# Kernel optimization log

Hardware: AMD Instinct MI355X
Metric: run time of the kernel (lower is better)

Reference implementation:

```python
import jax, jax.numpy as jnp
import numpy as np


def setup_inputs() -> dict:
    key = jax.random.key(0)
    kK, kV, kQ, kP, kA = jax.random.split(key, 5)
    b, d, N, T = 16, 512, 1024, 2048
    K = jax.random.normal(kK, (b, d, N), dtype=jnp.float32)
    V = jax.random.normal(kV, (b, d, N), dtype=jnp.float32)
    Q = jax.random.normal(kQ, (b, d, T), dtype=jnp.float32)
    previous_position = jax.random.randint(kP, (b,), 0, N)
    # previous attention: a valid attention matrix (softmax over N)
    previous_att = jax.nn.softmax(jax.random.uniform(kA, (b, N, T), dtype=jnp.float32), axis=1)
    return {
        "K": K,
        "V": V,
        "Q": Q,
        "force_incremental": 1,   # static python int -> bool branch
        "previous_position": previous_position,
        "previous_att": previous_att,
        "current_time": 1024,     # static python int timestep
    }


def reference(K, V, Q, force_incremental, previous_position, previous_att, current_time):
    # K, V: [b, d, N]; Q: [b, d, T]
    d = Q.shape[1]
    scale = 1.0 / np.sqrt(d)  # Config.d == feature dim
    # A: [b, N, T], softmax over N (text axis)
    A = jax.nn.softmax(jnp.einsum('bdn,bdt->bnt', K, Q) * scale, axis=1)
    current_position = jnp.argmax(A[:, :, current_time], axis=1)  # [b]
    if force_incremental:
        N = A.shape[1]
        # restore already-committed alignment prefix
        A = A.at[:, :, :current_time].set(previous_att[:, :, :current_time])
        difference = current_position - previous_position
        force_needed = (difference < -1) | (difference > 3)  # [b]
        # delta: one-hot at previous_position+1 (scatter_ of ones collapses to one-hot)
        idx = jnp.clip(previous_position + 1, 0, N - 1)
        delta = jax.nn.one_hot(idx, N, dtype=A.dtype)  # [b, N]
        col = jnp.where(force_needed[:, None], delta, A[:, :, current_time])
        A = A.at[:, :, current_time].set(col)
        current_position = jnp.argmax(col, axis=1)
    # R: [b, d, T]
    R = jnp.einsum('bdn,bnt->bdt', V, A)
    return A, R, current_position
```

## Files before the change

kernel.cpp:

```cpp
#include <hip/hip_runtime.h>
#include <hip/hip_bf16.h>

#define B_  16
#define D_  512
#define N_  1024
#define T_  2048
#define CT_ 1024
#define SCALE 0.04419417382415922f

typedef __attribute__((ext_vector_type(8))) short bf16x8;
typedef __attribute__((ext_vector_type(4))) float f32x4;
typedef __attribute__((ext_vector_type(8))) unsigned short u16x8;

#define GLDS16(g, l) __builtin_amdgcn_global_load_lds( \
    (const __attribute__((address_space(1))) unsigned int*)(g), \
    (__attribute__((address_space(3))) unsigned int*)(l), 16, 0, 0)

__device__ __forceinline__ unsigned short f2bf(float f) {
    union { float f; unsigned u; } v; v.f = f;
    unsigned r = v.u + 0x7fffu + ((v.u >> 16) & 1u);
    return (unsigned short)(r >> 16);
}
__device__ __forceinline__ float bf2f(unsigned short s) {
    union { unsigned u; float f; } v; v.u = ((unsigned)s) << 16;
    return v.f;
}


__global__ __launch_bounds__(256) void prep_all(
    const float* __restrict__ K, const float* __restrict__ Q,
    const float* __restrict__ V, const float* __restrict__ prev_att,
    unsigned short* __restrict__ KT, unsigned short* __restrict__ QT,
    unsigned short* __restrict__ Vbf, float* __restrict__ A,
    unsigned short* __restrict__ PbfT, float* __restrict__ invsum,
    float* __restrict__ colS) {
    __shared__ float tl[64][65];
    __shared__ float qv_s[64];
    __shared__ float red[256];
    const int bid = blockIdx.x;
    const int tid = threadIdx.x;
    const int rr = tid >> 4, cc = (tid & 15) * 4;

    if (bid < 4096) {
        const int nx = bid & 15, rem = bid >> 4;
        const int ty_ = rem & 15, b = rem >> 4;
        const int n0 = nx * 64, t0 = ty_ * 64;
        const float* ib = prev_att + (long)b * N_ * T_;
        float* Ab = A + (long)b * N_ * T_;
        unsigned short* ob = PbfT + (long)b * T_ * N_;
        f32x4 v[4];
#pragma unroll
        for (int p = 0; p < 4; ++p)
            v[p] = __builtin_nontemporal_load(
                (const f32x4*)&ib[(long)(n0 + p * 16 + rr) * T_ + t0 + cc]);
#pragma unroll
        for (int p = 0; p < 4; ++p)
            __builtin_nontemporal_store(
                v[p], (f32x4*)&Ab[(long)(n0 + p * 16 + rr) * T_ + t0 + cc]);
#pragma unroll
        for (int p = 0; p < 4; ++p) {
            tl[p*16+rr][cc] = v[p][0]; tl[p*16+rr][cc+1] = v[p][1];
            tl[p*16+rr][cc+2] = v[p][2]; tl[p*16+rr][cc+3] = v[p][3];
        }
        __syncthreads();
#pragma unroll
        for (int p = 0; p < 4; ++p) {
            int c = p * 16 + rr;
            ushort4 w;
            w.x = f2bf(tl[cc+0][c]); w.y = f2bf(tl[cc+1][c]);
            w.z = f2bf(tl[cc+2][c]); w.w = f2bf(tl[cc+3][c]);
            *(ushort4*)&ob[(long)(t0 + c) * N_ + n0 + cc] = w;
        }
    } else if (bid < 6144) {
        const int r = bid - 4096;
        const int rx = r & 7, rem = r >> 3;
        const int cy = rem & 15, b = rem >> 4;
        const int r0 = rx * 64, c0 = cy * 64;
        const float* ib = K + (long)b * D_ * N_;
        unsigned short* ob = KT + (long)b * 1024 * 512;
        if (tid < 64)
            qv_s[tid] = __builtin_nontemporal_load(
                &Q[((long)b * D_ + r0 + tid) * T_ + CT_]);
        f32x4 v[4];
#pragma unroll
        for (int p = 0; p < 4; ++p)
            v[p] = __builtin_nontemporal_load(
                (const f32x4*)&ib[(long)(r0 + p * 16 + rr) * N_ + c0 + cc]);
#pragma unroll
        for (int p = 0; p < 4; ++p) {
            tl[p*16+rr][cc] = v[p][0]; tl[p*16+rr][cc+1] = v[p][1];
            tl[p*16+rr][cc+2] = v[p][2]; tl[p*16+rr][cc+3] = v[p][3];
        }
        __syncthreads();
#pragma unroll
        for (int p = 0; p < 4; ++p) {
            int c = p * 16 + rr;
            ushort4 w;
            w.x = f2bf(tl[cc+0][c]); w.y = f2bf(tl[cc+1][c]);
            w.z = f2bf(tl[cc+2][c]); w.w = f2bf(tl[cc+3][c]);
            *(ushort4*)&ob[(long)(c0 + c) * 512 + r0 + cc] = w;
        }
        {
            const int n = tid & 63, g = tid >> 6;
            float p = 0.f;
#pragma unroll
            for (int j = 0; j < 16; ++j)
                p += tl[g * 16 + j][n] * qv_s[g * 16 + j];
            red[tid] = p;
            __syncthreads();
            if (tid < 64)
                atomicAdd(&colS[(long)b * N_ + c0 + tid],
                          red[tid] + red[64 + tid] + red[128 + tid] + red[192 + tid]);
        }
    } else if (bid < 8192) {
        const int r = bid - 6144;
        const int rx = r & 7, rem = r >> 3;
        const int cy = rem & 15, b = rem >> 4;
        const int r0 = rx * 64, c0 = cy * 64;
        const float* ib = Q + (long)b * D_ * T_;
        unsigned short* ob = QT + (long)b * 1024 * 512;
        f32x4 v[4];
#pragma unroll
        for (int p = 0; p < 4; ++p)
            v[p] = __builtin_nontemporal_load(
                (const f32x4*)&ib[(long)(r0 + p * 16 + rr) * T_ + CT_ + c0 + cc]);
#pragma unroll
        for (int p = 0; p < 4; ++p) {
            tl[p*16+rr][cc] = v[p][0]; tl[p*16+rr][cc+1] = v[p][1];
            tl[p*16+rr][cc+2] = v[p][2]; tl[p*16+rr][cc+3] = v[p][3];
        }
        __syncthreads();
#pragma unroll
        for (int p = 0; p < 4; ++p) {
            int c = p * 16 + rr;
            ushort4 w;
            w.x = f2bf(tl[cc+0][c]); w.y = f2bf(tl[cc+1][c]);
            w.z = f2bf(tl[cc+2][c]); w.w = f2bf(tl[cc+3][c]);
            *(ushort4*)&ob[(long)(c0 + c) * 512 + r0 + cc] = w;
        }
    } else if (bid < 9216) {
        const long total = (long)B_ * D_ * N_ / 4;
        for (long i = (long)(bid - 8192) * 256 + tid; i < total; i += 1024L * 256) {
            f32x4 v = __builtin_nontemporal_load(&((const f32x4*)V)[i]);
            ushort4 w;
            w.x = f2bf(v[0]); w.y = f2bf(v[1]); w.z = f2bf(v[2]); w.w = f2bf(v[3]);
            ((ushort4*)Vbf)[i] = w;
        }
    } else {
        const int idx = (bid - 9216) * 256 + tid;
        const int b = idx >> 10, t = idx & 1023;
        invsum[(long)b * T_ + t] = 1.0f;
    }
}

__global__ __launch_bounds__(256) void score_gemm_fused(
    const unsigned short* __restrict__ KT, const unsigned short* __restrict__ QT,
    unsigned short* __restrict__ PbfT, float* __restrict__ partial) {
    const int wg = blockIdx.x;
    const int b  = wg >> 6;
    const int rem = wg & 63;
    const int by = rem >> 3;
    const int bx = rem & 7;
    const int m0 = by * 128;
    const int t0 = bx * 128;
    __shared__ __align__(16) unsigned short buf[128 * 136];
    __shared__ float csum[2][128];
    unsigned short* sA = buf;
    unsigned short* sB = buf + 128 * 64;
    const int tid = threadIdx.x, lane = tid & 63, wave = tid >> 6;
    const int wm = wave >> 1, wn = wave & 1;
    const int lq = lane & 15, half = lane >> 4;
    const int srow = tid >> 3;
    const int cin  = tid & 7;

    const unsigned short* Ab = KT + (long)b * N_ * 512;
    const unsigned short* Bb = QT + (long)b * N_ * 512;

    f32x4 acc[4][4];
#pragma unroll
    for (int i = 0; i < 4; ++i)
#pragma unroll
        for (int j = 0; j < 4; ++j) acc[i][j] = f32x4{0.f, 0.f, 0.f, 0.f};

    for (int k0 = 0; k0 < 512; k0 += 64) {
#pragma unroll
        for (int c = 0; c < 4; ++c) {
            const int row  = c * 32 + srow;
            const int clog = cin ^ (row & 7);
            GLDS16(Ab + (long)(m0 + row) * 512 + k0 + clog * 8,
                   &sA[(c * 256 + wave * 64) * 8]);
            GLDS16(Bb + (long)(t0 + row) * 512 + k0 + clog * 8,
                   &sB[(c * 256 + wave * 64) * 8]);
        }
        __syncthreads();
#pragma unroll
        for (int kk = 0; kk < 2; ++kk) {
            bf16x8 af[4], bfr[4];
#pragma unroll
            for (int mi = 0; mi < 4; ++mi) {
                const int row = wm * 64 + mi * 16 + lq;
                af[mi] = *(const bf16x8*)&sA[row * 64 + (((kk * 4 + half) ^ (row & 7)) * 8)];
            }
#pragma unroll
            for (int ni = 0; ni < 4; ++ni) {
                const int row = wn * 64 + ni * 16 + lq;
                bfr[ni] = *(const bf16x8*)&sB[row * 64 + (((kk * 4 + half) ^ (row & 7)) * 8)];
            }
#pragma unroll
            for (int mi = 0; mi < 4; ++mi)
#pragma unroll
                for (int ni = 0; ni < 4; ++ni)
                    acc[mi][ni] = __builtin_amdgcn_mfma_f32_16x16x32_bf16(
                        af[mi], bfr[ni], acc[mi][ni], 0, 0, 0);
        }
        __syncthreads();
    }

#pragma unroll
    for (int mi = 0; mi < 4; ++mi)
#pragma unroll
        for (int ni = 0; ni < 4; ++ni)
#pragma unroll
            for (int r = 0; r < 4; ++r)
                acc[mi][ni][r] = __expf(acc[mi][ni][r] * SCALE);

    float cp[4];
#pragma unroll
    for (int ni = 0; ni < 4; ++ni) {
        float s = 0.f;
#pragma unroll
        for (int mi = 0; mi < 4; ++mi)
#pragma unroll
            for (int r = 0; r < 4; ++r) s += acc[mi][ni][r];
        s += __shfl_xor(s, 16);
        s += __shfl_xor(s, 32);
        cp[ni] = s;
    }

#pragma unroll
    for (int mi = 0; mi < 4; ++mi)
#pragma unroll
        for (int ni = 0; ni < 4; ++ni) {
            const int col = wn * 64 + ni * 16 + lq;
            const int row = wm * 64 + mi * 16 + half * 4;
            ushort4 w;
            w.x = f2bf(acc[mi][ni][0]); w.y = f2bf(acc[mi][ni][1]);
            w.z = f2bf(acc[mi][ni][2]); w.w = f2bf(acc[mi][ni][3]);
            *(ushort4*)&buf[col * 136 + row] = w;
        }
    if (lane < 16) {
#pragma unroll
        for (int ni = 0; ni < 4; ++ni)
            csum[wm][wn * 64 + ni * 16 + lane] = cp[ni];
    }
    __syncthreads();

    if (tid < 128)
        partial[((long)b * 8 + by) * 1024 + t0 + tid] =
            csum[0][tid] + csum[1][tid];

    unsigned short* ob = PbfT + (long)b * T_ * N_;
#pragma unroll
    for (int p = 0; p < 8; ++p) {
        const int idx = tid + p * 256;
        const int row = idx >> 4, ch = idx & 15;
        u16x8 w = *(const u16x8*)&buf[row * 136 + ch * 8];
        *(u16x8*)&ob[(long)(CT_ + t0 + row) * N_ + m0 + ch * 8] = w;
    }
}

__global__ __launch_bounds__(256) void emitA_inv(
    const unsigned short* __restrict__ PbfT, float* __restrict__ A,
    const float* __restrict__ partial, float* __restrict__ invsum) {
    const int b   = blockIdx.z;
    const int n0  = blockIdx.x * 64;
    const int tc0 = blockIdx.y * 128;
    __shared__ float tl[128][65];
    __shared__ float inv_s[128];
    const int tid = threadIdx.x;
    if (tid < 128) {
        float s = 0.f;
#pragma unroll
        for (int k = 0; k < 8; ++k) s += partial[((long)b * 8 + k) * 1024 + tc0 + tid];
        const float iv = 1.f / s;
        inv_s[tid] = iv;
        if (blockIdx.x == 0) invsum[(long)b * T_ + CT_ + tc0 + tid] = iv;
    }
    __syncthreads();
    const unsigned short* Pb = PbfT + (long)b * T_ * N_;
    float* Ab = A + (long)b * N_ * T_;
    const int rr = tid >> 4, cc = (tid & 15) * 4;
#pragma unroll
    for (int p = 0; p < 8; ++p) {
        const int row = p * 16 + rr;
        ushort4 w = *(const ushort4*)&Pb[(long)(CT_ + tc0 + row) * N_ + n0 + cc];
        const float inv = inv_s[row];
        tl[row][cc]   = bf2f(w.x) * inv; tl[row][cc+1] = bf2f(w.y) * inv;
        tl[row][cc+2] = bf2f(w.z) * inv; tl[row][cc+3] = bf2f(w.w) * inv;
    }
    __syncthreads();
    const int rr2 = tid >> 5, cc2 = (tid & 31) * 4;
#pragma unroll
    for (int p = 0; p < 8; ++p) {
        const int c = p * 8 + rr2;
        f32x4 o;
        o[0] = tl[cc2+0][c]; o[1] = tl[cc2+1][c];
        o[2] = tl[cc2+2][c]; o[3] = tl[cc2+3][c];
        __builtin_nontemporal_store(o, (f32x4*)&Ab[(long)(n0 + c) * T_ + CT_ + tc0 + cc2]);
    }
}

__global__ __launch_bounds__(256) void r_gemm_new(
    const unsigned short* __restrict__ Vbf, const unsigned short* __restrict__ PbfT,
    const float* __restrict__ invsum, float* __restrict__ R) {
    const int wg = blockIdx.x;
    const int b  = wg >> 6;
    const int rem = wg & 63;
    const int by = rem >> 4;
    const int bx = rem & 15;
    const int m0  = by * 128;
    const int nn0 = bx * 128;
    __shared__ __align__(16) unsigned short sA[128 * 64];
    __shared__ __align__(16) unsigned short sB[128 * 64];
    const int tid = threadIdx.x, lane = tid & 63, wave = tid >> 6;
    const int wm = wave >> 1, wn = wave & 1;
    const int lq = lane & 15, half = lane >> 4;
    const int srow = tid >> 3;
    const int cin  = tid & 7;

    const unsigned short* Ab = Vbf  + (long)b * D_ * N_;
    const unsigned short* Bb = PbfT + (long)b * T_ * N_;

    f32x4 acc[4][4];
#pragma unroll
    for (int i = 0; i < 4; ++i)
#pragma unroll
        for (int j = 0; j < 4; ++j) acc[i][j] = f32x4{0.f, 0.f, 0.f, 0.f};

    for (int k0 = 0; k0 < 1024; k0 += 64) {
#pragma unroll
        for (int c = 0; c < 4; ++c) {
            const int row  = c * 32 + srow;
            const int clog = cin ^ (row & 7);
            GLDS16(Ab + (long)(m0  + row) * 1024 + k0 + clog * 8,
                   &sA[(c * 256 + wave * 64) * 8]);
            GLDS16(Bb + (long)(nn0 + row) * 1024 + k0 + clog * 8,
                   &sB[(c * 256 + wave * 64) * 8]);
        }
        __syncthreads();
#pragma unroll
        for (int kk = 0; kk < 2; ++kk) {
            bf16x8 af[4], bfr[4];
#pragma unroll
            for (int mi = 0; mi < 4; ++mi) {
                const int row = wm * 64 + mi * 16 + lq;
                af[mi] = *(const bf16x8*)&sA[row * 64 + (((kk * 4 + half) ^ (row & 7)) * 8)];
            }
#pragma unroll
            for (int ni = 0; ni < 4; ++ni) {
                const int row = wn * 64 + ni * 16 + lq;
                bfr[ni] = *(const bf16x8*)&sB[row * 64 + (((kk * 4 + half) ^ (row & 7)) * 8)];
            }
#pragma unroll
            for (int mi = 0; mi < 4; ++mi)
#pragma unroll
                for (int ni = 0; ni < 4; ++ni)
                    acc[mi][ni] = __builtin_amdgcn_mfma_f32_16x16x32_bf16(
                        af[mi], bfr[ni], acc[mi][ni], 0, 0, 0);
        }
        __syncthreads();
    }
    float* Rb = R + (long)b * D_ * T_;
#pragma unroll
    for (int ni = 0; ni < 4; ++ni) {
        const int col = nn0 + wn * 64 + ni * 16 + lq;
        const float inv = invsum[(long)b * T_ + col];
#pragma unroll
        for (int mi = 0; mi < 4; ++mi)
#pragma unroll
            for (int r = 0; r < 4; ++r) {
                const int row = m0 + wm * 64 + mi * 16 + half * 4 + r;
                __builtin_nontemporal_store(acc[mi][ni][r] * inv,
                                            &Rb[(long)row * T_ + col]);
            }
    }
}

__global__ void col_scores_fp32(const float* __restrict__ K, const float* __restrict__ Q,
                                float* __restrict__ A) {
    const int b  = blockIdx.y;
    const int n0 = blockIdx.x * 128;
    const int tid = threadIdx.x;
    const int nl = tid & 127, dh = tid >> 7;
    __shared__ float qv[D_];
    __shared__ float part[256];
    for (int d = tid; d < D_; d += 256) qv[d] = Q[((long)b * D_ + d) * T_ + CT_];
    __syncthreads();
    float acc = 0.f;
    const float* Kb = K + (long)b * D_ * N_;
    for (int d = dh * 256; d < dh * 256 + 256; ++d)
        acc += Kb[(long)d * N_ + n0 + nl] * qv[d];
    part[tid] = acc;
    __syncthreads();
    if (tid < 128) {
        float s = (part[tid] + part[tid + 128]) * SCALE;
        A[((long)b * N_ + n0 + nl) * T_ + CT_] = s;
    }
}

__global__ void finalize_col(float* __restrict__ A, unsigned short* __restrict__ abfT,
                             float* __restrict__ invsum, const float* __restrict__ colS,
                             float* __restrict__ pos_out,
                             const int* __restrict__ prev_pos,
                             const int* __restrict__ force_p) {
    const int force = *force_p;
    const int b = blockIdx.x;
    const int tid = threadIdx.x;
    float* Ab = A + (long)b * N_ * T_;
    __shared__ float s[N_];
    __shared__ float redf[256];
    __shared__ int   redi[256];

    if (colS) {
        for (int n = tid; n < N_; n += 256) s[n] = colS[(long)b * N_ + n] * SCALE;
    } else {
        for (int n = tid; n < N_; n += 256) s[n] = Ab[(long)n * T_ + CT_];
    }
    __syncthreads();

    float m = -1e30f;
    for (int n = tid; n < N_; n += 256) m = fmaxf(m, s[n]);
    redf[tid] = m; __syncthreads();
    for (int w = 128; w > 0; w >>= 1) {
        if (tid < w) redf[tid] = fmaxf(redf[tid], redf[tid + w]);
        __syncthreads();
    }
    m = redf[0];
    __syncthreads();

    float sum = 0.f;
    for (int n = tid; n < N_; n += 256) sum += __expf(s[n] - m);
    redf[tid] = sum; __syncthreads();
    for (int w = 128; w > 0; w >>= 1) {
        if (tid < w) redf[tid] += redf[tid + w];
        __syncthreads();
    }
    sum = redf[0];
    __syncthreads();

    int idxl = N_;
    for (int n = tid; n < N_; n += 256) if (s[n] == m && n < idxl) idxl = n;
    redi[tid] = idxl; __syncthreads();
    for (int w = 128; w > 0; w >>= 1) {
        if (tid < w) redi[tid] = min(redi[tid], redi[tid + w]);
        __syncthreads();
    }
    const int cpos = redi[0];

    const int prev = prev_pos[b];
    const int diff = cpos - prev;
    const int fneed = force && (diff < -1 || diff > 3);
    int oneidx = prev + 1;
    oneidx = oneidx < 0 ? 0 : (oneidx > N_ - 1 ? N_ - 1 : oneidx);
    const float inv = 1.f / sum;

    for (int n = tid; n < N_; n += 256) {
        float v = fneed ? (n == oneidx ? 1.f : 0.f) : __expf(s[n] - m) * inv;
        Ab[(long)n * T_ + CT_] = v;
        if (abfT) abfT[(long)b * T_ * N_ + (long)CT_ * N_ + n] = f2bf(v);
    }
    if (tid == 0) {
        if (invsum) invsum[(long)b * T_ + CT_] = 1.0f;
        pos_out[b] = (float)(fneed ? oneidx : cpos);
    }
}

__global__ void copy_prefix(const float* __restrict__ prev_att, float* __restrict__ A) {
    const int per_row = CT_ >> 2;
    const long total = (long)B_ * N_ * per_row;
    for (long i = (long)blockIdx.x * blockDim.x + threadIdx.x; i < total;
         i += (long)gridDim.x * blockDim.x) {
        long row = i / per_row;
        int  c4  = (int)(i - row * per_row);
        long off = row * T_ + (long)c4 * 4;
        *(float4*)(A + off) = *(const float4*)(prev_att + off);
    }
}

__global__ void softmax_part_old(const float* __restrict__ A, float* __restrict__ partial) {
    const int b  = blockIdx.z;
    const int n0 = blockIdx.y * 128;
    const int tx = threadIdx.x & 63, ty = threadIdx.x >> 6;
    const int ci = blockIdx.x * 64 + tx;
    const int t  = CT_ + ci;
    const float* Ab = A + (long)b * N_ * T_;
    float s = 0.f;
    for (int r = ty; r < 128; r += 4)
        s += __expf(Ab[(long)(n0 + r) * T_ + t] * SCALE);
    __shared__ float red2[4][64];
    red2[ty][tx] = s;
    __syncthreads();
    if (ty == 0) {
        float tot = red2[0][tx] + red2[1][tx] + red2[2][tx] + red2[3][tx];
        partial[((long)b * 8 + blockIdx.y) * 1024 + ci] = tot;
    }
}

__global__ __launch_bounds__(256) void score_gemm_old(
    const float* __restrict__ K, const float* __restrict__ Q, float* __restrict__ A) {
    const int b  = blockIdx.z;
    const int n0 = blockIdx.y * 128;
    const int t0 = blockIdx.x * 128;
    __shared__ __align__(16) unsigned short sK[128 * 40];
    __shared__ __align__(16) unsigned short sQ[128 * 40];
    const int tid = threadIdx.x;
    const int lane = tid & 63, wave = tid >> 6;
    const int wm = wave >> 1, wn = wave & 1;
    const int lq = lane & 15, half = lane >> 4;
    const int xl = tid & 127, grp = tid >> 7;
    f32x4 acc[4][4];
#pragma unroll
    for (int i = 0; i < 4; ++i)
#pragma unroll
        for (int j = 0; j < 4; ++j) acc[i][j] = f32x4{0.f, 0.f, 0.f, 0.f};
    const float* Kb = K + (long)b * D_ * N_;
    const float* Qb = Q + (long)b * D_ * T_;
    for (int d0 = 0; d0 < D_; d0 += 32) {
#pragma unroll
        for (int j = 0; j < 4; ++j) {
            ushort4 w;
#pragma unroll
            for (int i = 0; i < 4; ++i)
                ((unsigned short*)&w)[i] = f2bf(Kb[(long)(d0 + grp*16 + j*4 + i) * N_ + n0 + xl]);
            *(ushort4*)&sK[xl * 40 + grp * 16 + j * 4] = w;
        }
#pragma unroll
        for (int j = 0; j < 4; ++j) {
            ushort4 w;
#pragma unroll
            for (int i = 0; i < 4; ++i)
                ((unsigned short*)&w)[i] = f2bf(Qb[(long)(d0 + grp*16 + j*4 + i) * T_ + CT_ + t0 + xl]);
            *(ushort4*)&sQ[xl * 40 + grp * 16 + j * 4] = w;
        }
        __syncthreads();
        bf16x8 af[4], bfr[4];
#pragma unroll
        for (int mi = 0; mi < 4; ++mi)
            af[mi] = *(const bf16x8*)&sK[(wm * 64 + mi * 16 + lq) * 40 + half * 8];
#pragma unroll
        for (int ni = 0; ni < 4; ++ni)
            bfr[ni] = *(const bf16x8*)&sQ[(wn * 64 + ni * 16 + lq) * 40 + half * 8];
#pragma unroll
        for (int mi = 0; mi < 4; ++mi)
#pragma unroll
            for (int ni = 0; ni < 4; ++ni)
                acc[mi][ni] = __builtin_amdgcn_mfma_f32_16x16x32_bf16(
                    af[mi], bfr[ni], acc[mi][ni], 0, 0, 0);
        __syncthreads();
    }
    float* Ab = A + (long)b * N_ * T_;
#pragma unroll
    for (int mi = 0; mi < 4; ++mi)
#pragma unroll
        for (int ni = 0; ni < 4; ++ni) {
            const int col = CT_ + t0 + wn * 64 + ni * 16 + lq;
#pragma unroll
            for (int r = 0; r < 4; ++r)
                Ab[(long)(n0 + wm*64 + mi*16 + half*4 + r) * T_ + col] = acc[mi][ni][r];
        }
}

__global__ void softmax_scale_old(float* __restrict__ A, const float* __restrict__ partial) {
    const int b  = blockIdx.z;
    const int n0 = blockIdx.y * 256;
    const int tx = threadIdx.x & 63, ty = threadIdx.x >> 6;
    const int ci = blockIdx.x * 64 + tx;
    const int t  = CT_ + ci;
    float sum = 0.f;
#pragma unroll
    for (int k = 0; k < 8; ++k) sum += partial[((long)b * 8 + k) * 1024 + ci];
    const float inv = 1.f / sum;
    float* Ab = A + (long)b * N_ * T_;
    for (int r = ty; r < 256; r += 4) {
        long off = (long)(n0 + r) * T_ + t;
        Ab[off] = __expf(Ab[off] * SCALE) * inv;
    }
}

__global__ __launch_bounds__(256) void r_gemm_old(
    const float* __restrict__ V, const float* __restrict__ A, float* __restrict__ R) {
    const int b  = blockIdx.z;
    const int d0 = blockIdx.y * 128;
    const int t0 = blockIdx.x * 128;
    __shared__ __align__(16) unsigned short sV[128 * 40];
    __shared__ __align__(16) unsigned short sA2[128 * 40];
    const int tid = threadIdx.x;
    const int lane = tid & 63, wave = tid >> 6;
    const int wm = wave >> 1, wn = wave & 1;
    const int lq = lane & 15, half = lane >> 4;
    const int xl = tid & 127, grp = tid >> 7;
    const int vd = tid >> 3, vn4 = (tid & 7) * 4;
    f32x4 acc[4][4];
#pragma unroll
    for (int i = 0; i < 4; ++i)
#pragma unroll
        for (int j = 0; j < 4; ++j) acc[i][j] = f32x4{0.f, 0.f, 0.f, 0.f};
    const float* Vb = V + (long)b * D_ * N_;
    const float* Ab = A + (long)b * N_ * T_;
    for (int n0 = 0; n0 < N_; n0 += 32) {
#pragma unroll
        for (int p = 0; p < 4; ++p) {
            int dl = p * 32 + vd;
            float4 v = *(const float4*)&Vb[(long)(d0 + dl) * N_ + n0 + vn4];
            ushort4 w;
            w.x = f2bf(v.x); w.y = f2bf(v.y); w.z = f2bf(v.z); w.w = f2bf(v.w);
            *(ushort4*)&sV[dl * 40 + vn4] = w;
        }
#pragma unroll
        for (int j = 0; j < 4; ++j) {
            ushort4 w;
#pragma unroll
            for (int i = 0; i < 4; ++i)
                ((unsigned short*)&w)[i] = f2bf(Ab[(long)(n0 + grp*16 + j*4 + i) * T_ + t0 + xl]);
            *(ushort4*)&sA2[xl * 40 + grp * 16 + j * 4] = w;
        }
        __syncthreads();
        bf16x8 af[4], bfr[4];
#pragma unroll
        for (int mi = 0; mi < 4; ++mi)
            af[mi] = *(const bf16x8*)&sV[(wm * 64 + mi * 16 + lq) * 40 + half * 8];
#pragma unroll
        for (int ni = 0; ni < 4; ++ni)
            bfr[ni] = *(const bf16x8*)&sA2[(wn * 64 + ni * 16 + lq) * 40 + half * 8];
#pragma unroll
        for (int mi = 0; mi < 4; ++mi)
#pragma unroll
            for (int ni = 0; ni < 4; ++ni)
                acc[mi][ni] = __builtin_amdgcn_mfma_f32_16x16x32_bf16(
                    af[mi], bfr[ni], acc[mi][ni], 0, 0, 0);
        __syncthreads();
    }
    float* Rb = R + (long)b * D_ * T_;
#pragma unroll
    for (int mi = 0; mi < 4; ++mi)
#pragma unroll
        for (int ni = 0; ni < 4; ++ni) {
            const int col = t0 + wn * 64 + ni * 16 + lq;
#pragma unroll
            for (int r = 0; r < 4; ++r)
                Rb[(long)(d0 + wm*64 + mi*16 + half*4 + r) * T_ + col] = acc[mi][ni][r];
        }
}

extern "C" void kernel_launch(void* const* d_in, const int* in_sizes, int n_in,
                              void* d_out, int out_size, void* d_ws, size_t ws_size,
                              hipStream_t stream) {
    const float* K        = (const float*)d_in[0];
    const float* V        = (const float*)d_in[1];
    const float* Q        = (const float*)d_in[2];
    const int*   force_p  = (const int*)d_in[3];
    const int*   prev_pos = (const int*)d_in[4];
    const float* prev_att = (const float*)d_in[5];

    float* A       = (float*)d_out;
    float* R       = A + (long)B_ * N_ * T_;
    float* pos_out = R + (long)B_ * D_ * T_;

    const size_t oKT = 0;
    const size_t oQT = oKT + (size_t)B_ * N_ * D_ * 2;
    const size_t oV  = oQT + (size_t)B_ * N_ * D_ * 2;
    const size_t oPT = oV  + (size_t)B_ * D_ * N_ * 2;
    const size_t oP  = oPT + (size_t)B_ * T_ * N_ * 2;
    const size_t oI  = oP  + (size_t)B_ * 8 * 1024 * 4;
    const size_t oCS = oI  + (size_t)B_ * T_ * 4;
    const size_t need = oCS + (size_t)B_ * N_ * 4;

    float* partial = (float*)((char*)d_ws + (ws_size >= need ? oP : 0));

    if (ws_size >= need) {
        unsigned short* KT   = (unsigned short*)((char*)d_ws + oKT);
        unsigned short* QT   = (unsigned short*)((char*)d_ws + oQT);
        unsigned short* Vbf  = (unsigned short*)((char*)d_ws + oV);
        unsigned short* PbfT = (unsigned short*)((char*)d_ws + oPT);
        float*          invs = (float*)((char*)d_ws + oI);
        float*          colS = (float*)((char*)d_ws + oCS);

        hipMemsetAsync(colS, 0, (size_t)B_ * N_ * 4, stream);
        prep_all        <<<9280, 256, 0, stream>>>(K, Q, V, prev_att,
                                                   KT, QT, Vbf, A, PbfT, invs, colS);
        score_gemm_fused<<<1024, 256, 0, stream>>>(KT, QT, PbfT, partial);
        emitA_inv       <<<dim3(16, 8, B_), 256, 0, stream>>>(PbfT, A, partial, invs);
        finalize_col    <<<B_, 256, 0, stream>>>(A, PbfT, invs, colS, pos_out,
                                                 prev_pos, force_p);
        r_gemm_new      <<<1024, 256, 0, stream>>>(Vbf, PbfT, invs, R);
    } else {
        copy_prefix       <<<2048, 256, 0, stream>>>(prev_att, A);
        score_gemm_old    <<<dim3(8, 8, B_), 256, 0, stream>>>(K, Q, A);
        softmax_part_old  <<<dim3(16, 8, B_), 256, 0, stream>>>(A, partial);
        softmax_scale_old <<<dim3(16, 4, B_), 256, 0, stream>>>(A, partial);
        col_scores_fp32   <<<dim3(8, B_), 256, 0, stream>>>(K, Q, A);
        finalize_col      <<<B_, 256, 0, stream>>>(A, (unsigned short*)nullptr,
                                                   (float*)nullptr, (const float*)nullptr,
                                                   pos_out, prev_pos, force_p);
        r_gemm_old        <<<dim3(16, 4, B_), 256, 0, stream>>>(V, A, R);
    }
}
```

Baseline: 166.6 us.

## Fuse A-emission into R GEMM launch and replace colS atomics with partials

The column-score reduction in prep_all now writes per-block partial sums instead of atomics, so the memset is dropped. finalize_all now also computes the inverse softmax sums. The separate emitA_inv kernel is folded into the R GEMM launch as extra blocks. This removes two launches and a memset, and lets the memory-bound A write run alongside the MFMA GEMM. In exchange, the fused kernel shares one LDS allocation and its two block types are heterogeneous, which may hurt occupancy or scheduling balance.

Result: no change. 164.5 us, median of 2 (-1.3%).

```diff
diff --git a/kernel.cpp b/kernel.cpp
--- a/kernel.cpp
+++ b/kernel.cpp
@@ -33,7 +33,7 @@
     unsigned short* __restrict__ KT, unsigned short* __restrict__ QT,
     unsigned short* __restrict__ Vbf, float* __restrict__ A,
     unsigned short* __restrict__ PbfT, float* __restrict__ invsum,
-    float* __restrict__ colS) {
+    float* __restrict__ colS_part) {
     __shared__ float tl[64][65];
     __shared__ float qv_s[64];
     __shared__ float red[256];
@@ -109,8 +109,8 @@
             red[tid] = p;
             __syncthreads();
             if (tid < 64)
-                atomicAdd(&colS[(long)b * N_ + c0 + tid],
-                          red[tid] + red[64 + tid] + red[128 + tid] + red[192 + tid]);
+                colS_part[((long)b * 8 + rx) * 1024 + c0 + tid] =
+                    red[tid] + red[64 + tid] + red[128 + tid] + red[192 + tid];
         }
     } else if (bid < 8192) {
         const int r = bid - 6144;
@@ -269,147 +269,10 @@
     }
 }
 
-__global__ __launch_bounds__(256) void emitA_inv(
-    const unsigned short* __restrict__ PbfT, float* __restrict__ A,
-    const float* __restrict__ partial, float* __restrict__ invsum) {
-    const int b   = blockIdx.z;
-    const int n0  = blockIdx.x * 64;
-    const int tc0 = blockIdx.y * 128;
-    __shared__ float tl[128][65];
-    __shared__ float inv_s[128];
-    const int tid = threadIdx.x;
-    if (tid < 128) {
-        float s = 0.f;
-#pragma unroll
-        for (int k = 0; k < 8; ++k) s += partial[((long)b * 8 + k) * 1024 + tc0 + tid];
-        const float iv = 1.f / s;
-        inv_s[tid] = iv;
-        if (blockIdx.x == 0) invsum[(long)b * T_ + CT_ + tc0 + tid] = iv;
-    }
-    __syncthreads();
-    const unsigned short* Pb = PbfT + (long)b * T_ * N_;
-    float* Ab = A + (long)b * N_ * T_;
-    const int rr = tid >> 4, cc = (tid & 15) * 4;
-#pragma unroll
-    for (int p = 0; p < 8; ++p) {
-        const int row = p * 16 + rr;
-        ushort4 w = *(const ushort4*)&Pb[(long)(CT_ + tc0 + row) * N_ + n0 + cc];
-        const float inv = inv_s[row];
-        tl[row][cc]   = bf2f(w.x) * inv; tl[row][cc+1] = bf2f(w.y) * inv;
-        tl[row][cc+2] = bf2f(w.z) * inv; tl[row][cc+3] = bf2f(w.w) * inv;
-    }
-    __syncthreads();
-    const int rr2 = tid >> 5, cc2 = (tid & 31) * 4;
-#pragma unroll
-    for (int p = 0; p < 8; ++p) {
-        const int c = p * 8 + rr2;
-        f32x4 o;
-        o[0] = tl[cc2+0][c]; o[1] = tl[cc2+1][c];
-        o[2] = tl[cc2+2][c]; o[3] = tl[cc2+3][c];
-        __builtin_nontemporal_store(o, (f32x4*)&Ab[(long)(n0 + c) * T_ + CT_ + tc0 + cc2]);
-    }
-}
-
-__global__ __launch_bounds__(256) void r_gemm_new(
-    const unsigned short* __restrict__ Vbf, const unsigned short* __restrict__ PbfT,
-    const float* __restrict__ invsum, float* __restrict__ R) {
-    const int wg = blockIdx.x;
-    const int b  = wg >> 6;
-    const int rem = wg & 63;
-    const int by = rem >> 4;
-    const int bx = rem & 15;
-    const int m0  = by * 128;
-    const int nn0 = bx * 128;
-    __shared__ __align__(16) unsigned short sA[128 * 64];
-    __shared__ __align__(16) unsigned short sB[128 * 64];
-    const int tid = threadIdx.x, lane = tid & 63, wave = tid >> 6;
-    const int wm = wave >> 1, wn = wave & 1;
-    const int lq = lane & 15, half = lane >> 4;
-    const int srow = tid >> 3;
-    const int cin  = tid & 7;
-
-    const unsigned short* Ab = Vbf  + (long)b * D_ * N_;
-    const unsigned short* Bb = PbfT + (long)b * T_ * N_;
-
-    f32x4 acc[4][4];
-#pragma unroll
-    for (int i = 0; i < 4; ++i)
-#pragma unroll
-        for (int j = 0; j < 4; ++j) acc[i][j] = f32x4{0.f, 0.f, 0.f, 0.f};
-
-    for (int k0 = 0; k0 < 1024; k0 += 64) {
-#pragma unroll
-        for (int c = 0; c < 4; ++c) {
-            const int row  = c * 32 + srow;
-            const int clog = cin ^ (row & 7);
-            GLDS16(Ab + (long)(m0  + row) * 1024 + k0 + clog * 8,
-                   &sA[(c * 256 + wave * 64) * 8]);
-            GLDS16(Bb + (long)(nn0 + row) * 1024 + k0 + clog * 8,
-                   &sB[(c * 256 + wave * 64) * 8]);
-        }
-        __syncthreads();
-#pragma unroll
-        for (int kk = 0; kk < 2; ++kk) {
-            bf16x8 af[4], bfr[4];
-#pragma unroll
-            for (int mi = 0; mi < 4; ++mi) {
-                const int row = wm * 64 + mi * 16 + lq;
-                af[mi] = *(const bf16x8*)&sA[row * 64 + (((kk * 4 + half) ^ (row & 7)) * 8)];
-            }
-#pragma unroll
-            for (int ni = 0; ni < 4; ++ni) {
-                const int row = wn * 64 + ni * 16 + lq;
-                bfr[ni] = *(const bf16x8*)&sB[row * 64 + (((kk * 4 + half) ^ (row & 7)) * 8)];
-            }
-#pragma unroll
-            for (int mi = 0; mi < 4; ++mi)
-#pragma unroll
-                for (int ni = 0; ni < 4; ++ni)
-                    acc[mi][ni] = __builtin_amdgcn_mfma_f32_16x16x32_bf16(
-                        af[mi], bfr[ni], acc[mi][ni], 0, 0, 0);
-        }
-        __syncthreads();
-    }
-    float* Rb = R + (long)b * D_ * T_;
-#pragma unroll
-    for (int ni = 0; ni < 4; ++ni) {
-        const int col = nn0 + wn * 64 + ni * 16 + lq;
-        const float inv = invsum[(long)b * T_ + col];
-#pragma unroll
-        for (int mi = 0; mi < 4; ++mi)
-#pragma unroll
-            for (int r = 0; r < 4; ++r) {
-                const int row = m0 + wm * 64 + mi * 16 + half * 4 + r;
-                __builtin_nontemporal_store(acc[mi][ni][r] * inv,
-                                            &Rb[(long)row * T_ + col]);
-            }
-    }
-}
-
-__global__ void col_scores_fp32(const float* __restrict__ K, const float* __restrict__ Q,
-                                float* __restrict__ A) {
-    const int b  = blockIdx.y;
-    const int n0 = blockIdx.x * 128;
-    const int tid = threadIdx.x;
-    const int nl = tid & 127, dh = tid >> 7;
-    __shared__ float qv[D_];
-    __shared__ float part[256];
-    for (int d = tid; d < D_; d += 256) qv[d] = Q[((long)b * D_ + d) * T_ + CT_];
-    __syncthreads();
-    float acc = 0.f;
-    const float* Kb = K + (long)b * D_ * N_;
-    for (int d = dh * 256; d < dh * 256 + 256; ++d)
-        acc += Kb[(long)d * N_ + n0 + nl] * qv[d];
-    part[tid] = acc;
-    __syncthreads();
-    if (tid < 128) {
-        float s = (part[tid] + part[tid + 128]) * SCALE;
-        A[((long)b * N_ + n0 + nl) * T_ + CT_] = s;
-    }
-}
-
-__global__ void finalize_col(float* __restrict__ A, unsigned short* __restrict__ abfT,
-                             float* __restrict__ invsum, const float* __restrict__ colS,
+__global__ void finalize_all(float* __restrict__ A, unsigned short* __restrict__ PbfT,
+                             float* __restrict__ invsum,
+                             const float* __restrict__ colS_part,
+                             const float* __restrict__ partial,
                              float* __restrict__ pos_out,
                              const int* __restrict__ prev_pos,
                              const int* __restrict__ force_p) {
@@ -421,10 +284,18 @@
     __shared__ float redf[256];
     __shared__ int   redi[256];
 
-    if (colS) {
-        for (int n = tid; n < N_; n += 256) s[n] = colS[(long)b * N_ + n] * SCALE;
-    } else {
-        for (int n = tid; n < N_; n += 256) s[n] = Ab[(long)n * T_ + CT_];
+    for (int t = tid; t < 1024; t += 256) {
+        float sm = 0.f;
+#pragma unroll
+        for (int k = 0; k < 8; ++k) sm += partial[((long)b * 8 + k) * 1024 + t];
+        invsum[(long)b * T_ + CT_ + t] = 1.f / sm;
+    }
+
+    for (int n = tid; n < N_; n += 256) {
+        float v = 0.f;
+#pragma unroll
+        for (int k = 0; k < 8; ++k) v += colS_part[((long)b * 8 + k) * 1024 + n];
+        s[n] = v * SCALE;
     }
     __syncthreads();
 
@@ -467,11 +338,124 @@
     for (int n = tid; n < N_; n += 256) {
         float v = fneed ? (n == oneidx ? 1.f : 0.f) : __expf(s[n] - m) * inv;
         Ab[(long)n * T_ + CT_] = v;
-        if (abfT) abfT[(long)b * T_ * N_ + (long)CT_ * N_ + n] = f2bf(v);
+        PbfT[(long)b * T_ * N_ + (long)CT_ * N_ + n] = f2bf(v);
     }
     if (tid == 0) {
-        if (invsum) invsum[(long)b * T_ + CT_] = 1.0f;
+        invsum[(long)b * T_ + CT_] = 1.0f;
         pos_out[b] = (float)(fneed ? oneidx : cpos);
+    }
+}
+
+__global__ __launch_bounds__(256) void rgemm_emitA(
+    const unsigned short* __restrict__ Vbf, const unsigned short* __restrict__ PbfT,
+    const float* __restrict__ invsum, float* __restrict__ R, float* __restrict__ A) {
+    __shared__ __align__(16) unsigned char smem[33792];
+    const int tid = threadIdx.x;
+
+    if (blockIdx.x < 1024) {
+        unsigned short* sA = (unsigned short*)smem;
+        unsigned short* sB = (unsigned short*)(smem + 16384);
+        const int wg = blockIdx.x;
+        const int b  = wg >> 6;
+        const int rem = wg & 63;
+        const int by = rem >> 4;
+        const int bx = rem & 15;
+        const int m0  = by * 128;
+        const int nn0 = bx * 128;
+        const int lane = tid & 63, wave = tid >> 6;
+        const int wm = wave >> 1, wn = wave & 1;
+        const int lq = lane & 15, half = lane >> 4;
+        const int srow = tid >> 3;
+        const int cin  = tid & 7;
+
+        const unsigned short* Ab = Vbf  + (long)b * D_ * N_;
+        const unsigned short* Bb = PbfT + (long)b * T_ * N_;
+
+        f32x4 acc[4][4];
+#pragma unroll
+        for (int i = 0; i < 4; ++i)
+#pragma unroll
+            for (int j = 0; j < 4; ++j) acc[i][j] = f32x4{0.f, 0.f, 0.f, 0.f};
+
+        for (int k0 = 0; k0 < 1024; k0 += 64) {
+#pragma unroll
+            for (int c = 0; c < 4; ++c) {
+                const int row  = c * 32 + srow;
+                const int clog = cin ^ (row & 7);
+                GLDS16(Ab + (long)(m0  + row) * 1024 + k0 + clog * 8,
+                       &sA[(c * 256 + wave * 64) * 8]);
+                GLDS16(Bb + (long)(nn0 + row) * 1024 + k0 + clog * 8,
+                       &sB[(c * 256 + wave * 64) * 8]);
+            }
+            __syncthreads();
+#pragma unroll
+            for (int kk = 0; kk < 2; ++kk) {
+                bf16x8 af[4], bfr[4];
+#pragma unroll
+                for (int mi = 0; mi < 4; ++mi) {
+                    const int row = wm * 64 + mi * 16 + lq;
+                    af[mi] = *(const bf16x8*)&sA[row * 64 + (((kk * 4 + half) ^ (row & 7)) * 8)];
+                }
+#pragma unroll
+                for (int ni = 0; ni < 4; ++ni) {
+                    const int row = wn * 64 + ni * 16 + lq;
+                    bfr[ni] = *(const bf16x8*)&sB[row * 64 + (((kk * 4 + half) ^ (row & 7)) * 8)];
+                }
+#pragma unroll
+                for (int mi = 0; mi < 4; ++mi)
+#pragma unroll
+                    for (int ni = 0; ni < 4; ++ni)
+                        acc[mi][ni] = __builtin_amdgcn_mfma_f32_16x16x32_bf16(
+                            af[mi], bfr[ni], acc[mi][ni], 0, 0, 0);
+            }
+            __syncthreads();
+        }
+        float* Rb = R + (long)b * D_ * T_;
+#pragma unroll
+        for (int ni = 0; ni < 4; ++ni) {
+            const int col = nn0 + wn * 64 + ni * 16 + lq;
+            const float inv = invsum[(long)b * T_ + col];
+#pragma unroll
+            for (int mi = 0; mi < 4; ++mi)
+#pragma unroll
+                for (int r = 0; r < 4; ++r) {
+                    const int row = m0 + wm * 64 + mi * 16 + half * 4 + r;
+                    __builtin_nontemporal_store(acc[mi][ni][r] * inv,
+                                                &Rb[(long)row * T_ + col]);
+                }
+        }
+    } else {
+        float (*tl)[65] = (float(*)[65])smem;
+        float* inv_s = (float*)(smem + 33280);
+        const int r = blockIdx.x - 1024;
+        const int n0x = r & 15, rem = r >> 4;
+        const int tcy = rem & 7, b = rem >> 3;
+        const int n0  = n0x * 64;
+        const int tc0 = tcy * 128;
+        if (tid < 128) inv_s[tid] = invsum[(long)b * T_ + CT_ + tc0 + tid];
+        __syncthreads();
+        const unsigned short* Pb = PbfT + (long)b * T_ * N_;
+        float* Ab = A + (long)b * N_ * T_;
+        const int rr = tid >> 4, cc = (tid & 15) * 4;
+#pragma unroll
+        for (int p = 0; p < 8; ++p) {
+            const int row = p * 16 + rr;
+            ushort4 w = *(const ushort4*)&Pb[(long)(CT_ + tc0 + row) * N_ + n0 + cc];
+            const float inv = inv_s[row];
+            tl[row][cc]   = bf2f(w.x) * inv; tl[row][cc+1] = bf2f(w.y) * inv;
+            tl[row][cc+2] = bf2f(w.z) * inv; tl[row][cc+3] = bf2f(w.w) * inv;
+        }
+        __syncthreads();
+        const int rr2 = tid >> 5, cc2 = (tid & 31) * 4;
+#pragma unroll
+        for (int p = 0; p < 8; ++p) {
+            const int c = p * 8 + rr2;
+            f32x4 o;
+            o[0] = tl[cc2+0][c]; o[1] = tl[cc2+1][c];
+            o[2] = tl[cc2+2][c]; o[3] = tl[cc2+3][c];
+            __builtin_nontemporal_store(
+                o, (f32x4*)&Ab[(long)(n0 + c) * T_ + CT_ + tc0 + cc2]);
+        }
     }
 }
 
@@ -585,6 +569,80 @@
         long off = (long)(n0 + r) * T_ + t;
         Ab[off] = __expf(Ab[off] * SCALE) * inv;
     }
+}
+
+__global__ void col_scores_fp32(const float* __restrict__ K, const float* __restrict__ Q,
+                                float* __restrict__ A) {
+    const int b  = blockIdx.y;
+    const int n0 = blockIdx.x * 128;
+    const int tid = threadIdx.x;
+    const int nl = tid & 127, dh = tid >> 7;
+    __shared__ float qv[D_];
+    __shared__ float part[256];
+    for (int d = tid; d < D_; d += 256) qv[d] = Q[((long)b * D_ + d) * T_ + CT_];
+    __syncthreads();
+    float acc = 0.f;
+    const float* Kb = K + (long)b * D_ * N_;
+    for (int d = dh * 256; d < dh * 256 + 256; ++d)
+        acc += Kb[(long)d * N_ + n0 + nl] * qv[d];
+    part[tid] = acc;
+    __syncthreads();
+    if (tid < 128) {
+        float s = (part[tid] + part[tid + 128]) * SCALE;
+        A[((long)b * N_ + n0 + nl) * T_ + CT_] = s;
+    }
+}
+
+__global__ void finalize_col_old(float* __restrict__ A, float* __restrict__ pos_out,
+                                 const int* __restrict__ prev_pos,
+                                 const int* __restrict__ force_p) {
+    const int force = *force_p;
+    const int b = blockIdx.x;
+    const int tid = threadIdx.x;
+    float* Ab = A + (long)b * N_ * T_;
+    __shared__ float s[N_];
+    __shared__ float redf[256];
+    __shared__ int   redi[256];
+
+    for (int n = tid; n < N_; n += 256) s[n] = Ab[(long)n * T_ + CT_];
+    __syncthreads();
+    float m = -1e30f;
+    for (int n = tid; n < N_; n += 256) m = fmaxf(m, s[n]);
+    redf[tid] = m; __syncthreads();
+    for (int w = 128; w > 0; w >>= 1) {
+        if (tid < w) redf[tid] = fmaxf(redf[tid], redf[tid + w]);
+        __syncthreads();
+    }
+    m = redf[0];
+    __syncthreads();
+    float sum = 0.f;
+    for (int n = tid; n < N_; n += 256) sum += __expf(s[n] - m);
+    redf[tid] = sum; __syncthreads();
+    for (int w = 128; w > 0; w >>= 1) {
+        if (tid < w) redf[tid] += redf[tid + w];
+        __syncthreads();
+    }
+    sum = redf[0];
+    __syncthreads();
+    int idxl = N_;
+    for (int n = tid; n < N_; n += 256) if (s[n] == m && n < idxl) idxl = n;
+    redi[tid] = idxl; __syncthreads();
+    for (int w = 128; w > 0; w >>= 1) {
+        if (tid < w) redi[tid] = min(redi[tid], redi[tid + w]);
+        __syncthreads();
+    }
+    const int cpos = redi[0];
+    const int prev = prev_pos[b];
+    const int diff = cpos - prev;
+    const int fneed = force && (diff < -1 || diff > 3);
+    int oneidx = prev + 1;
+    oneidx = oneidx < 0 ? 0 : (oneidx > N_ - 1 ? N_ - 1 : oneidx);
+    const float inv = 1.f / sum;
+    for (int n = tid; n < N_; n += 256) {
+        float v = fneed ? (n == oneidx ? 1.f : 0.f) : __expf(s[n] - m) * inv;
+        Ab[(long)n * T_ + CT_] = v;
+    }
+    if (tid == 0) pos_out[b] = (float)(fneed ? oneidx : cpos);
 }
 
 __global__ __launch_bounds__(256) void r_gemm_old(
@@ -672,8 +730,8 @@
     const size_t oPT = oV  + (size_t)B_ * D_ * N_ * 2;
     const size_t oP  = oPT + (size_t)B_ * T_ * N_ * 2;
     const size_t oI  = oP  + (size_t)B_ * 8 * 1024 * 4;
-    const size_t oCS = oI  + (size_t)B_ * T_ * 4;
-    const size_t need = oCS + (size_t)B_ * N_ * 4;
+    const size_t oCP = oI  + (size_t)B_ * T_ * 4;
+    const size_t need = oCP + (size_t)B_ * 8 * 1024 * 4;
 
     float* partial = (float*)((char*)d_ws + (ws_size >= need ? oP : 0));
 
@@ -683,25 +741,21 @@
         unsigned short* Vbf  = (unsigned short*)((char*)d_ws + oV);
         unsigned short* PbfT = (unsigned short*)((char*)d_ws + oPT);
         float*          invs = (float*)((char*)d_ws + oI);
-        float*          colS = (float*)((char*)d_ws + oCS);
-
-        hipMemsetAsync(colS, 0, (size_t)B_ * N_ * 4, stream);
+        float*          colP = (float*)((char*)d_ws + oCP);
+
         prep_all        <<<9280, 256, 0, stream>>>(K, Q, V, prev_att,
-                                                   KT, QT, Vbf, A, PbfT, invs, colS);
+                                                   KT, QT, Vbf, A, PbfT, invs, colP);
         score_gemm_fused<<<1024, 256, 0, stream>>>(KT, QT, PbfT, partial);
-        emitA_inv       <<<dim3(16, 8, B_), 256, 0, stream>>>(PbfT, A, partial, invs);
-        finalize_col    <<<B_, 256, 0, stream>>>(A, PbfT, invs, colS, pos_out,
-                                                 prev_pos, force_p);
-        r_gemm_new      <<<1024, 256, 0, stream>>>(Vbf, PbfT, invs, R);
+        finalize_all    <<<B_, 256, 0, stream>>>(A, PbfT, invs, colP, partial,
+                                                 pos_out, prev_pos, force_p);
+        rgemm_emitA     <<<3072, 256, 0, stream>>>(Vbf, PbfT, invs, R, A);
     } else {
         copy_prefix       <<<2048, 256, 0, stream>>>(prev_att, A);
         score_gemm_old    <<<dim3(8, 8, B_), 256, 0, stream>>>(K, Q, A);
         softmax_part_old  <<<dim3(16, 8, B_), 256, 0, stream>>>(A, partial);
         softmax_scale_old <<<dim3(16, 4, B_), 256, 0, stream>>>(A, partial);
         col_scores_fp32   <<<dim3(8, B_), 256, 0, stream>>>(K, Q, A);
-        finalize_col      <<<B_, 256, 0, stream>>>(A, (unsigned short*)nullptr,
-                                                   (float*)nullptr, (const float*)nullptr,
-                                                   pos_out, prev_pos, force_p);
+        finalize_col_old  <<<B_, 256, 0, stream>>>(A, pos_out, prev_pos, force_p);
         r_gemm_old        <<<dim3(16, 4, B_), 256, 0, stream>>>(V, A, R);
     }
 }
```
